# Optimization experiments

Hardware: AMD Instinct MI355X
Metric: run time of the kernel (lower is better)

## Reference

```python
import jax, jax.numpy as jnp
import numpy as np

B, F, C, W_, H_ = 4, 8, 256, 7, 7   # batch, frames, compressed channels (in_dim//r), width, height
CIN = 2048                          # in_dim
CH = CIN // 16                      # in_dim // (2*r) = 128, per-branch q/k channels


def _pw2d(x, W, b):
    # 1x1 Conv2d == per-pixel channel matmul. x: (N,Cin,H,W), W: (Cout,Cin)
    return jnp.einsum('nchw,oc->nohw', x, W) + b[None, :, None, None]


def setup_inputs() -> dict:
    key = jax.random.key(0)
    ks = iter(jax.random.split(key, 40))
    def rn(shape, s=0.02):
        return jax.random.normal(next(ks), shape, dtype=jnp.float32) * s
    inp = {
        'x':       rn((B * F, CIN, H_, W_), 1.0),
        'domainX': rn((B * F, CIN, H_, W_), 1.0),
        'domainY': rn((B * F, 1, H_, W_), 1.0),
        # conv1_1_pre (1 -> 2048), output is discarded in forward but computed faithfully
        'w_pre': rn((CIN, 1)), 'b_pre': rn((CIN,)),
        # conv3 (2048 -> 256); its weight is SHARED with layer1_downconv and layer1_downconv_Y
        'w_conv3': rn((C, CIN)), 'b_conv3': rn((C,)),
        # value_conv 1x1x1 Conv3d (256 -> 2048); weight SHARED with layer1_upconv(_Y)
        'w_value': rn((CIN, C)), 'b_value': rn((CIN,)),
        # tied-weight convs have their own biases
        'b_l1down': rn((C,)), 'b_l1up': rn((CIN,)),
        'b_l1down_Y': rn((C,)), 'b_l1up_Y': rn((CIN,)),
        # layer2 convs: independent weights (layer2_*gamma init to 0, so init add is a no-op)
        'w_l2down': rn((C, CIN)), 'b_l2down': rn((C,)),
        'w_l2up': rn((CIN, C)), 'b_l2up': rn((CIN,)),
        'w_l2down_Y': rn((C, CIN)), 'b_l2down_Y': rn((C,)),
        'w_l2up_Y': rn((CIN, C)), 'b_l2up_Y': rn((CIN,)),
        # q/k projections (2048 -> 128 each)
        'w_c11': rn((CH, CIN)), 'b_c11': rn((CH,)),
        'w_c12': rn((CH, CIN)), 'b_c12': rn((CH,)),
        'w_c21': rn((CH, CIN)), 'b_c21': rn((CH,)),
        'w_c22': rn((CH, CIN)), 'b_c22': rn((CH,)),
        'pos_embedV': rn((1, F, C * H_ * W_), 1.0),
        'gamma': jnp.asarray(0.01, dtype=jnp.float32),
    }
    return inp


def reference(x, domainX, domainY, w_pre, b_pre, w_conv3, b_conv3, w_value, b_value,
              b_l1down, b_l1up, b_l1down_Y, b_l1up_Y,
              w_l2down, b_l2down, w_l2up, b_l2up,
              w_l2down_Y, b_l2down_Y, w_l2up_Y, b_l2up_Y,
              w_c11, b_c11, w_c12, b_c12, w_c21, b_c21, w_c22, b_c22,
              pos_embedV, gamma):
    S = F * W_ * H_  # 392 tokens per clip
    # conv1_1_pre output is overwritten in the original forward (dead computation)
    _dead = _pw2d(domainY, w_pre, b_pre)
    del _dead
    # domainY path: down(conv3 weight) -> up(value_conv weight) -> layer2 down -> layer2 up
    # (create5D/create4D + permutes + 1x1x1 conv3d collapse to pointwise channel matmuls)
    dY = _pw2d(_pw2d(_pw2d(_pw2d(domainX, w_conv3, b_l1down_Y), w_value, b_l1up_Y),
                     w_l2down_Y, b_l2down_Y), w_l2up_Y, b_l2up_Y)
    q4 = jnp.concatenate([_pw2d(x, w_c11, b_c11), _pw2d(dY, w_c12, b_c12)], axis=1)  # (32,256,7,7)
    q = q4.reshape(B, F, C, W_, H_).transpose(0, 1, 3, 4, 2).reshape(B, S, C)
    # domainX path (same structure, shared layer1 weights, its own biases)
    dX = _pw2d(_pw2d(_pw2d(_pw2d(domainX, w_conv3, b_l1down), w_value, b_l1up),
                     w_l2down, b_l2down), w_l2up, b_l2up)
    k4 = jnp.concatenate([_pw2d(x, w_c21, b_c21), _pw2d(dX, w_c22, b_c22)], axis=1)
    k5 = k4.reshape(B, F, C, W_, H_).transpose(0, 1, 3, 4, 2)        # (B,F,W,H,C)
    k = k5.transpose(0, 2, 1, 3, 4).reshape(B, C, S)                 # faithful odd permute
    # value: conv3 -> +pos_embed -> rearrange to (B, S, C)
    v4 = _pw2d(x, w_conv3, b_conv3)                                  # (32,256,7,7)
    v = v4.reshape(B, F, C * W_ * H_) + pos_embedV                   # dropout p=0 is identity
    v = v.reshape(B, F, C, W_, H_).transpose(0, 1, 3, 4, 2).reshape(B, S, C)
    attn = jax.nn.softmax(jnp.einsum('bnc,bcm->bnm', q, k), axis=-1)  # (B,392,392)
    out = jnp.einsum('bnm,bmc->bnc', attn, v)
    out = out.reshape(B, F, W_, H_, C).transpose(0, 4, 1, 2, 3)      # (B,C,F,W,H)
    out = jnp.einsum('bcthw,oc->bothw', out, w_value) + b_value[None, :, None, None, None]
    out = out.transpose(0, 2, 1, 3, 4).reshape(B * F, CIN, W_, H_)
    return (gamma * out + x) * out + x
```

## Files before the change

### kernel.cpp

```cpp
#include <hip/hip_runtime.h>
#include <hip/hip_bf16.h>


typedef __attribute__((ext_vector_type(8))) short short8;
typedef __attribute__((ext_vector_type(4))) float f32x4;

#define TOKENS 1568

__device__ __forceinline__ ushort f2bf(float f) {
    uint32_t u = __float_as_uint(f);
    u += 0x7fffu + ((u >> 16) & 1u);
    return (ushort)(u >> 16);
}
__device__ __forceinline__ float bf2f(ushort h) { return __uint_as_float(((uint32_t)h) << 16); }
__device__ __forceinline__ void split2(float v, ushort& h, ushort& l) {
    h = f2bf(v); l = f2bf(v - bf2f(h));
}

__device__ __forceinline__ void gl16(const void* g, void* l) {
    __builtin_amdgcn_global_load_lds(
        (const __attribute__((address_space(1))) unsigned int*)g,
        (__attribute__((address_space(3))) unsigned int*)l, 16, 0, 0);
}

#define EPI_PART  0
#define EPI_BF16  1
#define EPI_SPLIT 2
#define EPI_FINAL 3

struct GA {
    const ushort *Ah, *Al; int lda; long sA;
    const ushort *Wh, *Wl; int ldw; long sW;
    const float* bias; int sB;
    int nkc, Kc;
    float* fO; ushort *bO, *bO2;
    int ldc; long sC; int M, N;
    int nx, ny;
    const float *ex, *gamma; float* fout;
};

template<int EPI, int SPL>
__device__ __forceinline__ void gmm_body(const GA g, int bx, int by, int bzf,
    ushort* LA_h, ushort* LW_h, ushort* LA_l, ushort* LW_l)
{
    constexpr bool HASL = (SPL >= 1);
    const int tid = threadIdx.x;
    const int bz = bzf / g.nkc;
    const int kc = bzf % g.nkc;
    const int row0 = by * 64, col0 = bx * 128;
    const bool sp = (SPL == 1) || (SPL == 2 && bx < 2);

    const int srow = tid >> 2;
    const int sq   = (tid & 3) ^ (srow & 3);
    int am  = row0 + srow;      if (am  > g.M - 1) am  = g.M - 1;
    int wn0 = col0 + srow;      if (wn0 > g.N - 1) wn0 = g.N - 1;
    int wn1 = col0 + 64 + srow; if (wn1 > g.N - 1) wn1 = g.N - 1;
    const long kbase = (long)kc * g.Kc + sq * 8;
    const ushort* gA  = g.Ah + bz * g.sA + (long)am  * g.lda + kbase;
    const ushort* gW0 = g.Wh + bz * g.sW + (long)wn0 * g.ldw + kbase;
    const ushort* gW1 = g.Wh + bz * g.sW + (long)wn1 * g.ldw + kbase;
    const ushort *gAl = nullptr, *gWl0 = nullptr, *gWl1 = nullptr;
    if constexpr (HASL) {
        if (sp) {
            gAl  = g.Al + bz * g.sA + (long)am  * g.lda + kbase;
            gWl0 = g.Wl + bz * g.sW + (long)wn0 * g.ldw + kbase;
            gWl1 = g.Wl + bz * g.sW + (long)wn1 * g.ldw + kbase;
        }
    }
    const int wb = (tid & 192) * 8;

    auto STAGE = [&](int buf, int k0) {
        gl16(gA + k0, LA_h + buf * 2048 + wb);
        gl16(gW0 + k0, LW_h + buf * 4096 + wb);
        gl16(gW1 + k0, LW_h + buf * 4096 + 2048 + wb);
        if constexpr (HASL) {
            if (sp) {
                gl16(gAl + k0, LA_l + buf * 2048 + wb);
                gl16(gWl0 + k0, LW_l + buf * 4096 + wb);
                gl16(gWl1 + k0, LW_l + buf * 4096 + 2048 + wb);
            }
        }
    };

    const int lane = tid & 63, wv = tid >> 6;
    const int wr = (wv >> 1) * 32, wc = (wv & 1) * 64;
    const int fr = lane & 15;
    const int ksw = ((lane >> 4) ^ (lane & 3)) * 8;
    int aoff[2], boff[4];
#pragma unroll
    for (int mi = 0; mi < 2; ++mi) aoff[mi] = (wr + mi * 16 + fr) * 32 + ksw;
#pragma unroll
    for (int ni = 0; ni < 4; ++ni) boff[ni] = (wc + ni * 16 + fr) * 32 + ksw;

    f32x4 acc[2][4];
#pragma unroll
    for (int mi = 0; mi < 2; ++mi)
#pragma unroll
        for (int ni = 0; ni < 4; ++ni) acc[mi][ni] = (f32x4){0.f, 0.f, 0.f, 0.f};

    STAGE(0, 0);
    __syncthreads();
    int cur = 0;
    for (int k0 = 0; k0 < g.Kc; k0 += 32) {
        if (k0 + 32 < g.Kc) STAGE(cur ^ 1, k0 + 32);

        short8 fa[2], fb[4];
#pragma unroll
        for (int mi = 0; mi < 2; ++mi) fa[mi] = *(const short8*)&LA_h[cur * 2048 + aoff[mi]];
#pragma unroll
        for (int ni = 0; ni < 4; ++ni) fb[ni] = *(const short8*)&LW_h[cur * 4096 + boff[ni]];
#pragma unroll
        for (int mi = 0; mi < 2; ++mi)
#pragma unroll
            for (int ni = 0; ni < 4; ++ni)
                acc[mi][ni] = __builtin_amdgcn_mfma_f32_16x16x32_bf16(fa[mi], fb[ni], acc[mi][ni], 0, 0, 0);
        if constexpr (HASL) {
            if (sp) {
                short8 ga[2], gb[4];
#pragma unroll
                for (int mi = 0; mi < 2; ++mi) ga[mi] = *(const short8*)&LA_l[cur * 2048 + aoff[mi]];
#pragma unroll
                for (int ni = 0; ni < 4; ++ni) gb[ni] = *(const short8*)&LW_l[cur * 4096 + boff[ni]];
#pragma unroll
                for (int mi = 0; mi < 2; ++mi)
#pragma unroll
                    for (int ni = 0; ni < 4; ++ni) {
                        acc[mi][ni] = __builtin_amdgcn_mfma_f32_16x16x32_bf16(fa[mi], gb[ni], acc[mi][ni], 0, 0, 0);
                        acc[mi][ni] = __builtin_amdgcn_mfma_f32_16x16x32_bf16(ga[mi], fb[ni], acc[mi][ni], 0, 0, 0);
                    }
            }
        }
        __syncthreads();
        cur ^= 1;
    }

    const int q4 = (lane >> 4) * 4;
    float gg = 0.f;
    if constexpr (EPI == EPI_FINAL) gg = g.gamma[0];
#pragma unroll
    for (int mi = 0; mi < 2; ++mi)
#pragma unroll
        for (int ni = 0; ni < 4; ++ni)
#pragma unroll
            for (int qi = 0; qi < 4; ++qi) {
                int m = row0 + wr + mi * 16 + q4 + qi;
                int n = col0 + wc + ni * 16 + fr;
                if (m >= g.M || n >= g.N) continue;
                float v = acc[mi][ni][qi];
                if (g.bias) v += g.bias[bz * g.sB + n];
                if constexpr (EPI == EPI_PART) {
                    g.fO[(long)bzf * g.sC + (long)m * g.ldc + n] = v;
                } else if constexpr (EPI == EPI_BF16) {
                    g.bO[(long)bzf * g.sC + (long)m * g.ldc + n] = f2bf(v);
                } else if constexpr (EPI == EPI_SPLIT) {
                    long o = (long)bzf * g.sC + (long)m * g.ldc + n;
                    ushort h, l; split2(v, h, l);
                    g.bO[o] = h; g.bO2[o] = l;
                } else {
                    int nimg = m / 49, p = m % 49;
                    long xi = (long)nimg * (2048 * 49) + (long)n * 49 + p;
                    float xv = g.ex[xi];
                    g.fout[xi] = (gg * v + xv) * v + xv;
                }
            }
}

template<int EPI, int SPL>
__global__ __launch_bounds__(256)
void gmm(GA g)
{
    __shared__ __align__(16) ushort LAh[2 * 2048], LWh[2 * 4096];
    __shared__ __align__(16) ushort LAl[(SPL >= 1) ? 2 * 2048 : 8];
    __shared__ __align__(16) ushort LWl[(SPL >= 1) ? 2 * 4096 : 8];
    gmm_body<EPI, SPL>(g, blockIdx.x, blockIdx.y, blockIdx.z, LAh, LWh, LAl, LWl);
}

template<int E1, int S1, int E2, int S2, int E3, int S3>
__global__ __launch_bounds__(256)
void gmm3(GA g1, int n1, GA g2, int n2, GA g3)
{
    __shared__ __align__(16) ushort LAh[2 * 2048], LWh[2 * 4096];
    __shared__ __align__(16) ushort LAl[2 * 2048], LWl[2 * 4096];
    int id = blockIdx.x;
    if (id < n1) {
        int bx = id % g1.nx, t = id / g1.nx;
        gmm_body<E1, S1>(g1, bx, t % g1.ny, t / g1.ny, LAh, LWh, LAl, LWl);
    } else if (id < n1 + n2) {
        id -= n1;
        int bx = id % g2.nx, t = id / g2.nx;
        gmm_body<E2, S2>(g2, bx, t % g2.ny, t / g2.ny, LAh, LWh, LAl, LWl);
    } else {
        id -= n1 + n2;
        int bx = id % g3.nx, t = id / g3.nx;
        gmm_body<E3, S3>(g3, bx, t % g3.ny, t / g3.ny, LAh, LWh, LAl, LWl);
    }
}

__global__ __launch_bounds__(256)
void prep(const float* c11, const float* c21, const float* conv3,
          const float* c22, const float* c12, const float* wval,
          const float* w2dX, const float* w2dY,
          const float* b_c11, const float* b_c21, const float* b_conv3,
          const float* x, const float* dX,
          const float* w2u, const float* w2uY, const float* wv, const float* w3,
          ushort* Wg1h, ushort* Wg1l, ushort* C2h, ushort* C2l, ushort* Wvalb,
          ushort* W2dSh, ushort* W2dSl, float* bg1,
          ushort* Xth, ushort* Xtl, ushort* DXth, ushort* DXtl,
          ushort* W2uTh, ushort* W2uTl, ushort* WvTh, ushort* WvTl,
          ushort* W3Th, ushort* W3Tl)
{
    __shared__ float tile[64][65];
    int b = blockIdx.x;
    int tid = threadIdx.x;
    if (b < 12290) {
        int e = b * 256 + tid;
        if (e < 1048576) {
            float v = e < 262144 ? c11[e] : e < 524288 ? c21[e - 262144] : conv3[e - 524288];
            ushort h, l; split2(v, h, l); Wg1h[e] = h; Wg1l[e] = l;
        } else if (e < 1572864) {
            int i = e - 1048576;
            float v = i < 262144 ? c22[i] : c12[i - 262144];
            ushort h, l; split2(v, h, l); C2h[i] = h; C2l[i] = l;
        } else if (e < 2097152) {
            int i = e - 1572864; Wvalb[i] = f2bf(wval[i]);
        } else if (e < 2097664) {
            int i = e - 2097152;
            bg1[i] = i < 128 ? b_c11[i] : i < 256 ? b_c21[i - 128] : b_conv3[i - 256];
        } else {
            int i = e - 2097664;
            float v = i < 524288 ? w2dX[i] : w2dY[i - 524288];
            ushort h, l; split2(v, h, l); W2dSh[i] = h; W2dSl[i] = l;
        }
    } else if (b < 14338) {
        int local = b - 12290;
        int z = local >> 10;
        int rem = local & 1023;
        int n = rem & 31, c0 = (rem >> 5) * 64;
        const float* src = z ? dX : x;
        ushort* oh = z ? DXth : Xth;
        ushort* ol = z ? DXtl : Xtl;
        const float* s = src + (long)n * (2048 * 49) + (long)c0 * 49;
        for (int idx = tid; idx < 64 * 49; idx += 256)
            tile[idx / 49][idx % 49] = s[idx];
        __syncthreads();
        for (int idx = tid; idx < 49 * 64; idx += 256) {
            int p = idx >> 6, cl = idx & 63;
            float v = tile[cl][p];
            long o = (long)(n * 49 + p) * 2048 + c0 + cl;
            ushort h, l; split2(v, h, l);
            oh[o] = h; ol[o] = l;
        }
    } else {
        int local = b - 14338;
        int zc = local >> 7, t = local & 127;
        const float* src; ushort *dh, *dl; int rows;
        switch (zc) {
            case 0:  src = w2u;  dh = W2uTh;          dl = W2uTl;          rows = 2048; break;
            case 1:  src = w2uY; dh = W2uTh + 524288; dl = W2uTl + 524288; rows = 2048; break;
            case 2:  src = wv;   dh = WvTh;           dl = WvTl;           rows = 2048; break;
            default: src = w3;   dh = W3Th;           dl = W3Tl;           rows = 256;  break;
        }
        int cols = 524288 / rows;
        int tilesX = cols >> 6;
        int tx = t % tilesX, ty = t / tilesX;
        for (int i = tid; i < 4096; i += 256) {
            int r = i >> 6, c = i & 63;
            tile[r][c] = src[(long)(ty * 64 + r) * cols + tx * 64 + c];
        }
        __syncthreads();
        for (int i = tid; i < 4096; i += 256) {
            int c = i >> 6, r = i & 63;
            float v = tile[r][c];
            ushort h, l; split2(v, h, l);
            long o = (long)(tx * 64 + c) * rows + ty * 64 + r;
            dh[o] = h; dl[o] = l;
        }
    }
}

__global__ __launch_bounds__(256)
void redA(const float* __restrict__ PG1, const float* __restrict__ bg1,
          const float* __restrict__ pos,
          ushort* Qh, ushort* Ql, ushort* KmH, ushort* KmL, ushort* Vh,
          const float* __restrict__ A1p, ushort* A1h, ushort* A1l,
          const float* __restrict__ Dp, ushort* DTh, ushort* DTl,
          const float* w2dX, const float* w2dY,
          const float* b1dX, const float* b1uX, const float* b2dX,
          const float* b1dY, const float* b1uY, const float* b2dY,
          float* __restrict__ dvec)
{
    int blk = blockIdx.x, tid = threadIdx.x;
    if (blk < 3136) {
        int idx = blk * 256 + tid;
        int m = idx >> 9, n = idx & 511;
        float v = bg1[n];
#pragma unroll
        for (int k = 0; k < 8; ++k) v += PG1[(long)k * 802816 + idx];
        int p = m % 49, img = m / 49;
        int f = img & 7, b = img >> 3;
        if (n < 128) {
            ushort h, l; split2(v, h, l);
            Qh[m * 256 + n] = h; Ql[m * 256 + n] = l;
        } else if (n < 256) {
            int c = n - 128;
            int flat = (p / 7) * 14336 + f * 1792 + (p % 7) * 256 + c;
            int ci = flat / 392, mm = flat % 392;
            long o = (long)b * 100352 + (long)mm * 256 + ci;
            ushort h, l; split2(v, h, l);
            KmH[o] = h; KmL[o] = l;
        } else {
            int c = n - 256;
            v += pos[f * 12544 + c * 49 + p];
            int s = m % 392;
            long o = (long)b * 106496 + (long)c * 416 + s;
            Vh[o] = f2bf(v);
            if (s < 24) Vh[o + 392] = 0;
        }
    } else if (blk < 3200) {
        int b2 = blk - 3136;
#pragma unroll
        for (int r = 0; r < 4; ++r) {
            int idx = b2 * 1024 + r * 256 + tid;
            int z = idx >> 15, e = idx & 32767;
            float v = 0.f;
#pragma unroll
            for (int k = 0; k < 8; ++k) v += A1p[(long)(z * 8 + k) * 32768 + e];
            ushort h, l; split2(v, h, l);
            A1h[idx] = h; A1l[idx] = l;
        }
    } else if (blk < 3232) {
        int b2 = blk - 3200;
#pragma unroll
        for (int r = 0; r < 16; ++r) {
            int idx = b2 * 4096 + r * 256 + tid;
            int z = idx >> 16, e = idx & 65535;
            int i = e >> 8, j = e & 255;
            float v = 0.f;
#pragma unroll
            for (int k = 0; k < 8; ++k) v += Dp[(long)(z * 8 + k) * 65536 + e];
            ushort h, l; split2(v, h, l);
            long o = (long)z * 65536 + (long)j * 256 + i;
            DTh[o] = h; DTl[o] = l;
        }
    } else {
        int blk2 = blk - 3232;
        int z = blk2 >> 6;
        int lane = tid & 63, wv = tid >> 6;
        int c = (blk2 & 63) * 4 + wv;
        const float* w2d = (z ? w2dY : w2dX) + (long)c * 2048;
        const float* b1d = z ? b1dY : b1dX;
        const float* b1u = z ? b1uY : b1uX;
        const float* b2d = z ? b2dY : b2dX;
        float acc = 0.f;
        for (int o = lane; o < 2048; o += 64) acc = fmaf(w2d[o], b1u[o], acc);
        for (int j = lane; j < 256; j += 64) {
            float d = 0.f;
#pragma unroll
            for (int k = 0; k < 8; ++k) d += Dp[(long)(z * 8 + k) * 65536 + (long)c * 256 + j];
            acc = fmaf(d, b1d[j], acc);
        }
        for (int off = 32; off; off >>= 1) acc += __shfl_down(acc, off, 64);
        if (lane == 0) dvec[z * 256 + c] = acc + b2d[c];
    }
}

__global__ __launch_bounds__(256)
void mkc(GA gM,
         const ushort* __restrict__ A1h, const ushort* __restrict__ A1l,
         const float* __restrict__ dvec,
         const float* c22, const float* c12,
         const float* b2uX, const float* b2uY,
         const float* bc22, const float* bc12, float* kc)
{
    __shared__ __align__(16) ushort LAh[2 * 2048], LWh[2 * 4096];
    __shared__ __align__(16) ushort LAl[2 * 2048], LWl[2 * 4096];
    int id = blockIdx.x;
    if (id < 64) {
        gmm_body<EPI_SPLIT, 1>(gM, id & 15, (id >> 4) & 1, id >> 5, LAh, LWh, LAl, LWl);
        return;
    }
    int tid = threadIdx.x, lane = tid & 63, wv = tid >> 6;
    int w = (id - 64) * 4 + wv;
    int z = w >> 7, i = w & 127;
    const ushort* a1h = A1h + (long)z * 32768 + i * 256;
    const ushort* a1l = A1h + (long)z * 32768 + i * 256;
    a1l = (const ushort*)((const ushort*)A1l + (long)z * 32768 + i * 256);
    const float* dv = dvec + z * 256;
    const float* cr = (z ? c12 : c22) + (long)i * 2048;
    const float* b2u = z ? b2uY : b2uX;
    float acc = 0.f;
    for (int c = lane; c < 256; c += 64)
        acc = fmaf(bf2f(a1h[c]) + bf2f(a1l[c]), dv[c], acc);
    for (int o = lane; o < 2048; o += 64) acc = fmaf(cr[o], b2u[o], acc);
    for (int off = 32; off; off >>= 1) acc += __shfl_down(acc, off, 64);
    if (lane == 0) kc[z * 128 + i] = acc + (z ? bc12 : bc22)[i];
}

__global__ __launch_bounds__(256)
void r_qk2(const float* __restrict__ P, const float* __restrict__ kc,
           ushort* Qh, ushort* Ql, ushort* KmH, ushort* KmL)
{
    int idx = blockIdx.x * 256 + threadIdx.x;
    int m = idx >> 8, j = idx & 255;
    float v = kc[j];
#pragma unroll
    for (int k = 0; k < 8; ++k) v += P[(long)k * 401408 + idx];
    ushort h, l; split2(v, h, l);
    if (j < 128) {
        int c = 128 + j;
        int p = m % 49, img = m / 49, f = img & 7, b = img >> 3;
        int flat = (p / 7) * 14336 + f * 1792 + (p % 7) * 256 + c;
        int ci = flat / 392, mm = flat % 392;
        long o = (long)b * 100352 + (long)mm * 256 + ci;
        KmH[o] = h; KmL[o] = l;
    } else {
        Qh[m * 256 + j] = h; Ql[m * 256 + j] = l;
    }
}

__global__ __launch_bounds__(256)
void fattn(const ushort* __restrict__ Qh, const ushort* __restrict__ Ql,
           const ushort* __restrict__ Kmh, const ushort* __restrict__ Kml,
           const ushort* __restrict__ VT, ushort* __restrict__ O)
{
    __shared__ float raw[16 * 420];
    __shared__ ushort P[16 * 424];
    const int b = blockIdx.y;
    const int r0 = blockIdx.x * 16;
    const int tid = threadIdx.x;
    const int lane = tid & 63, wv = tid >> 6;
    const int fr = lane & 15, g = lane >> 4;
    const int kb = g * 8;
    const long base = (long)b * 100352;
    const long vbase = (long)b * 106496;

    int qr = r0 + fr; if (qr > 391) qr = 391;
    const ushort* qph = Qh + base + (long)qr * 256 + kb;
    const ushort* qpl = Ql + base + (long)qr * 256 + kb;
    short8 qh[8], ql[8];
#pragma unroll
    for (int kf = 0; kf < 8; ++kf) {
        qh[kf] = *(const short8*)(qph + kf * 32);
        ql[kf] = *(const short8*)(qpl + kf * 32);
    }

    for (int nf = wv; nf < 26; nf += 4) {
        int kcol = nf * 16 + fr; if (kcol > 391) kcol = 391;
        const ushort* kph = Kmh + base + (long)kcol * 256 + kb;
        const ushort* kpl = Kml + base + (long)kcol * 256 + kb;
        f32x4 a = (f32x4){0.f, 0.f, 0.f, 0.f};
#pragma unroll
        for (int kf = 0; kf < 8; ++kf) {
            short8 bh = *(const short8*)(kph + kf * 32);
            short8 bl = *(const short8*)(kpl + kf * 32);
            a = __builtin_amdgcn_mfma_f32_16x16x32_bf16(qh[kf], bh, a, 0, 0, 0);
            a = __builtin_amdgcn_mfma_f32_16x16x32_bf16(qh[kf], bl, a, 0, 0, 0);
            a = __builtin_amdgcn_mfma_f32_16x16x32_bf16(ql[kf], bh, a, 0, 0, 0);
        }
#pragma unroll
        for (int q = 0; q < 4; ++q)
            raw[(g * 4 + q) * 420 + nf * 16 + fr] = a[q];
    }
    __syncthreads();

    {
        int row = tid >> 4, j = tid & 15;
        float v[26];
        float m = -1e30f;
#pragma unroll
        for (int k = 0; k < 26; ++k) {
            int col = j + 16 * k;
            v[k] = (col < 392) ? raw[row * 420 + col] : -1e30f;
            m = fmaxf(m, v[k]);
        }
#pragma unroll
        for (int off = 8; off; off >>= 1) m = fmaxf(m, __shfl_xor(m, off, 16));
        float s = 0.f;
#pragma unroll
        for (int k = 0; k < 26; ++k) { v[k] = __expf(v[k] - m); s += v[k]; }
#pragma unroll
        for (int off = 8; off; off >>= 1) s += __shfl_xor(s, off, 16);
        float inv = 1.f / s;
#pragma unroll
        for (int k = 0; k < 26; ++k) {
            int col = j + 16 * k;
            P[row * 424 + col] = (col < 392) ? f2bf(v[k] * inv) : (ushort)0;
        }
    }
    __syncthreads();

    const int cf0 = wv * 4;
    f32x4 o[4];
#pragma unroll
    for (int c = 0; c < 4; ++c) o[c] = (f32x4){0.f, 0.f, 0.f, 0.f};
#pragma unroll
    for (int kf = 0; kf < 13; ++kf) {
        short8 pa = *(const short8*)&P[fr * 424 + kf * 32 + kb];
#pragma unroll
        for (int c = 0; c < 4; ++c) {
            const ushort* vp = VT + vbase + (long)((cf0 + c) * 16 + fr) * 416 + kf * 32 + kb;
            short8 vb = *(const short8*)vp;
            o[c] = __builtin_amdgcn_mfma_f32_16x16x32_bf16(pa, vb, o[c], 0, 0, 0);
        }
    }
#pragma unroll
    for (int c = 0; c < 4; ++c)
#pragma unroll
        for (int q = 0; q < 4; ++q) {
            int orow = r0 + g * 4 + q;
            if (orow < 392)
                O[base + (long)orow * 256 + (cf0 + c) * 16 + fr] = f2bf(o[c][q]);
        }
}

extern "C" void kernel_launch(void* const* d_in, const int* in_sizes, int n_in,
                              void* d_out, int out_size, void* d_ws, size_t ws_size,
                              hipStream_t stream)
{
    const float* x        = (const float*)d_in[0];
    const float* domainX  = (const float*)d_in[1];
    const float* w_conv3  = (const float*)d_in[5];
    const float* b_conv3  = (const float*)d_in[6];
    const float* w_value  = (const float*)d_in[7];
    const float* b_value  = (const float*)d_in[8];
    const float* b_l1down   = (const float*)d_in[9];
    const float* b_l1up     = (const float*)d_in[10];
    const float* b_l1down_Y = (const float*)d_in[11];
    const float* b_l1up_Y   = (const float*)d_in[12];
    const float* w_l2down   = (const float*)d_in[13];
    const float* b_l2down   = (const float*)d_in[14];
    const float* w_l2up     = (const float*)d_in[15];
    const float* b_l2up     = (const float*)d_in[16];
    const float* w_l2down_Y = (const float*)d_in[17];
    const float* b_l2down_Y = (const float*)d_in[18];
    const float* w_l2up_Y   = (const float*)d_in[19];
    const float* b_l2up_Y   = (const float*)d_in[20];
    const float* w_c11 = (const float*)d_in[21];
    const float* b_c11 = (const float*)d_in[22];
    const float* w_c12 = (const float*)d_in[23];
    const float* b_c12 = (const float*)d_in[24];
    const float* w_c21 = (const float*)d_in[25];
    const float* b_c21 = (const float*)d_in[26];
    const float* w_c22 = (const float*)d_in[27];
    const float* b_c22 = (const float*)d_in[28];
    const float* pos   = (const float*)d_in[29];
    const float* gamma = (const float*)d_in[30];
    float* out = (float*)d_out;

    ushort* U = (ushort*)d_ws;
    float*  Fp = (float*)d_ws;

    const long oXt_h   = 0;
    const long oXt_l   = 3211264;
    const long oDXt_h  = 6422528;
    const long oDXt_l  = 9633792;
    const long oWg1_h  = 12845056;
    const long oWg1_l  = 13893632;
    const long oWval   = 14942208;
    const long oC2_h   = 15466496;
    const long oC2_l   = 15990784;
    const long oW2uT_h = 16515072;
    const long oW2uT_l = 17563648;
    const long oWvT_h  = 18612224;
    const long oWvT_l  = 19136512;
    const long oW3T_h  = 19660800;
    const long oW3T_l  = 20185088;
    const long oW2dS_h = 20709376;
    const long oW2dS_l = 21757952;
    const long oQ_h    = 22806528;
    const long oQ_l    = 23207936;
    const long oKm_h   = 23609344;
    const long oKm_l   = 24010752;
    const long oVT     = 24412160;
    const long oA1_h   = 24838144;
    const long oA1_l   = 24903680;
    const long oDT_h   = 24969216;
    const long oDT_l   = 25100288;
    const long oA3_h   = 25231360;
    const long oA3_l   = 25296896;
    const long oM_h    = 25362432;
    const long oM_l    = 25886720;
    const long oO      = 26411008;
    const long fPG1   = 13406208;
    const long fA1p   = 19828736;
    const long fDp    = 20353024;
    const long fPG2   = 21401600;
    const long fbg1   = 24612864;
    const long fkc    = 24613376;
    const long fdv    = 24613632;

    GA Z = {};

    prep<<<dim3(14850), 256, 0, stream>>>(
        w_c11, w_c21, w_conv3, w_c22, w_c12, w_value, w_l2down, w_l2down_Y,
        b_c11, b_c21, b_conv3, x, domainX,
        w_l2up, w_l2up_Y, w_value, w_conv3,
        U + oWg1_h, U + oWg1_l, U + oC2_h, U + oC2_l, U + oWval,
        U + oW2dS_h, U + oW2dS_l, Fp + fbg1,
        U + oXt_h, U + oXt_l, U + oDXt_h, U + oDXt_l,
        U + oW2uT_h, U + oW2uT_l, U + oWvT_h, U + oWvT_l,
        U + oW3T_h, U + oW3T_l);

    {
        GA g1 = Z;
        g1.Ah = U + oXt_h; g1.Al = U + oXt_l; g1.lda = 2048; g1.sA = 0;
        g1.Wh = U + oWg1_h; g1.Wl = U + oWg1_l; g1.ldw = 2048; g1.sW = 0;
        g1.nkc = 8; g1.Kc = 256; g1.fO = Fp + fPG1;
        g1.ldc = 512; g1.sC = 802816; g1.M = TOKENS; g1.N = 512; g1.nx = 4; g1.ny = 25;
        GA ga1 = Z;
        ga1.Ah = U + oC2_h; ga1.Al = U + oC2_l; ga1.lda = 2048; ga1.sA = 262144;
        ga1.Wh = U + oW2uT_h; ga1.Wl = U + oW2uT_l; ga1.ldw = 2048; ga1.sW = 524288;
        ga1.nkc = 8; ga1.Kc = 256; ga1.fO = Fp + fA1p;
        ga1.ldc = 256; ga1.sC = 32768; ga1.M = 128; ga1.N = 256; ga1.nx = 2; ga1.ny = 2;
        GA gd = Z;
        gd.Ah = U + oW2dS_h; gd.Al = U + oW2dS_l; gd.lda = 2048; gd.sA = 524288;
        gd.Wh = U + oWvT_h; gd.Wl = U + oWvT_l; gd.ldw = 2048; gd.sW = 0;
        gd.nkc = 8; gd.Kc = 256; gd.fO = Fp + fDp;
        gd.ldc = 256; gd.sC = 65536; gd.M = 256; gd.N = 256; gd.nx = 2; gd.ny = 4;
        gmm3<EPI_PART, 2, EPI_PART, 1, EPI_PART, 1><<<dim3(992), 256, 0, stream>>>(
            g1, 800, ga1, 64, gd);
    }

    redA<<<dim3(3360), 256, 0, stream>>>(Fp + fPG1, Fp + fbg1, pos,
        U + oQ_h, U + oQ_l, U + oKm_h, U + oKm_l, U + oVT,
        Fp + fA1p, U + oA1_h, U + oA1_l,
        Fp + fDp, U + oDT_h, U + oDT_l,
        w_l2down, w_l2down_Y,
        b_l1down, b_l1up, b_l2down,
        b_l1down_Y, b_l1up_Y, b_l2down_Y,
        Fp + fdv);

    {
        GA g = Z;
        g.Ah = U + oA1_h; g.Al = U + oA1_l; g.lda = 256; g.sA = 32768;
        g.Wh = U + oDT_h; g.Wl = U + oDT_l; g.ldw = 256; g.sW = 65536;
        g.nkc = 1; g.Kc = 256; g.bO = U + oA3_h; g.bO2 = U + oA3_l;
        g.ldc = 256; g.sC = 32768; g.M = 128; g.N = 256; g.nx = 2; g.ny = 2;
        gmm<EPI_SPLIT, 1><<<dim3(2, 2, 2), 256, 0, stream>>>(g);
    }

    {
        GA g = Z;
        g.Ah = U + oA3_h; g.Al = U + oA3_l; g.lda = 256; g.sA = 32768;
        g.Wh = U + oW3T_h; g.Wl = U + oW3T_l; g.ldw = 256; g.sW = 0;
        g.nkc = 1; g.Kc = 256; g.bO = U + oM_h; g.bO2 = U + oM_l;
        g.ldc = 2048; g.sC = 262144; g.M = 128; g.N = 2048; g.nx = 16; g.ny = 2;
        mkc<<<dim3(128), 256, 0, stream>>>(g,
            U + oA1_h, U + oA1_l, Fp + fdv,
            w_c22, w_c12, b_l2up, b_l2up_Y,
            b_c22, b_c12, Fp + fkc);
    }

    {
        GA g = Z;
        g.Ah = U + oDXt_h; g.Al = U + oDXt_l; g.lda = 2048; g.sA = 0;
        g.Wh = U + oM_h; g.Wl = U + oM_l; g.ldw = 2048; g.sW = 0;
        g.nkc = 8; g.Kc = 256; g.fO = Fp + fPG2;
        g.ldc = 256; g.sC = 401408; g.M = TOKENS; g.N = 256; g.nx = 2; g.ny = 25;
        gmm<EPI_PART, 1><<<dim3(2, 25, 8), 256, 0, stream>>>(g);
    }

    r_qk2<<<dim3(1568), 256, 0, stream>>>(Fp + fPG2, Fp + fkc,
        U + oQ_h, U + oQ_l, U + oKm_h, U + oKm_l);

    fattn<<<dim3(25, 4), 256, 0, stream>>>(
        U + oQ_h, U + oQ_l, U + oKm_h, U + oKm_l, U + oVT, U + oO);

    {
        GA g = Z;
        g.Ah = U + oO; g.Al = nullptr; g.lda = 256; g.sA = 0;
        g.Wh = U + oWval; g.Wl = nullptr; g.ldw = 256; g.sW = 0;
        g.bias = b_value; g.sB = 0;
        g.nkc = 1; g.Kc = 256;
        g.ldc = 0; g.sC = 0; g.M = TOKENS; g.N = 2048; g.nx = 16; g.ny = 25;
        g.ex = x; g.gamma = gamma; g.fout = out;
        gmm<EPI_FINAL, 0><<<dim3(16, 25, 1), 256, 0, stream>>>(g);
    }
}
```

Before: 170.6 us.

## Replace split-bf16 hi/lo emulation with single fp16 MFMA throughout pipeline

```diff
diff --git a/kernel.cpp b/kernel.cpp
--- a/kernel.cpp
+++ b/kernel.cpp
@@ -2,19 +2,18 @@
 #include <hip/hip_bf16.h>
 
 
-typedef __attribute__((ext_vector_type(8))) short short8;
+typedef __attribute__((ext_vector_type(8))) _Float16 half8;
 typedef __attribute__((ext_vector_type(4))) float f32x4;
 
 #define TOKENS 1568
 
-__device__ __forceinline__ ushort f2bf(float f) {
-    uint32_t u = __float_as_uint(f);
-    u += 0x7fffu + ((u >> 16) & 1u);
-    return (ushort)(u >> 16);
-}
-__device__ __forceinline__ float bf2f(ushort h) { return __uint_as_float(((uint32_t)h) << 16); }
-__device__ __forceinline__ void split2(float v, ushort& h, ushort& l) {
-    h = f2bf(v); l = f2bf(v - bf2f(h));
+__device__ __forceinline__ ushort f2h(float f) {
+    _Float16 h = (_Float16)f;
+    return *(ushort*)&h;
+}
+__device__ __forceinline__ float h2f(ushort u) {
+    _Float16 h = *(_Float16*)&u;
+    return (float)h;
 }
 
 __device__ __forceinline__ void gl16(const void* g, void* l) {
@@ -24,31 +23,28 @@
 }
 
 #define EPI_PART  0
-#define EPI_BF16  1
-#define EPI_SPLIT 2
-#define EPI_FINAL 3
+#define EPI_F16   1
+#define EPI_FINAL 2
 
 struct GA {
-    const ushort *Ah, *Al; int lda; long sA;
-    const ushort *Wh, *Wl; int ldw; long sW;
+    const ushort* Ah; int lda; long sA;
+    const ushort* Wh; int ldw; long sW;
     const float* bias; int sB;
     int nkc, Kc;
-    float* fO; ushort *bO, *bO2;
+    float* fO; ushort* bO;
     int ldc; long sC; int M, N;
     int nx, ny;
     const float *ex, *gamma; float* fout;
 };
 
-template<int EPI, int SPL>
+template<int EPI>
 __device__ __forceinline__ void gmm_body(const GA g, int bx, int by, int bzf,
-    ushort* LA_h, ushort* LW_h, ushort* LA_l, ushort* LW_l)
-{
-    constexpr bool HASL = (SPL >= 1);
+                                         ushort* LA, ushort* LW)
+{
     const int tid = threadIdx.x;
     const int bz = bzf / g.nkc;
     const int kc = bzf % g.nkc;
     const int row0 = by * 64, col0 = bx * 128;
-    const bool sp = (SPL == 1) || (SPL == 2 && bx < 2);
 
     const int srow = tid >> 2;
     const int sq   = (tid & 3) ^ (srow & 3);
@@ -59,27 +55,12 @@
     const ushort* gA  = g.Ah + bz * g.sA + (long)am  * g.lda + kbase;
     const ushort* gW0 = g.Wh + bz * g.sW + (long)wn0 * g.ldw + kbase;
     const ushort* gW1 = g.Wh + bz * g.sW + (long)wn1 * g.ldw + kbase;
-    const ushort *gAl = nullptr, *gWl0 = nullptr, *gWl1 = nullptr;
-    if constexpr (HASL) {
-        if (sp) {
-            gAl  = g.Al + bz * g.sA + (long)am  * g.lda + kbase;
-            gWl0 = g.Wl + bz * g.sW + (long)wn0 * g.ldw + kbase;
-            gWl1 = g.Wl + bz * g.sW + (long)wn1 * g.ldw + kbase;
-        }
-    }
     const int wb = (tid & 192) * 8;
 
     auto STAGE = [&](int buf, int k0) {
-        gl16(gA + k0, LA_h + buf * 2048 + wb);
-        gl16(gW0 + k0, LW_h + buf * 4096 + wb);
-        gl16(gW1 + k0, LW_h + buf * 4096 + 2048 + wb);
-        if constexpr (HASL) {
-            if (sp) {
-                gl16(gAl + k0, LA_l + buf * 2048 + wb);
-                gl16(gWl0 + k0, LW_l + buf * 4096 + wb);
-                gl16(gWl1 + k0, LW_l + buf * 4096 + 2048 + wb);
-            }
-        }
+        gl16(gA + k0, LA + buf * 2048 + wb);
+        gl16(gW0 + k0, LW + buf * 4096 + wb);
+        gl16(gW1 + k0, LW + buf * 4096 + 2048 + wb);
     };
 
     const int lane = tid & 63, wv = tid >> 6;
@@ -104,32 +85,16 @@
     for (int k0 = 0; k0 < g.Kc; k0 += 32) {
         if (k0 + 32 < g.Kc) STAGE(cur ^ 1, k0 + 32);
 
-        short8 fa[2], fb[4];
-#pragma unroll
-        for (int mi = 0; mi < 2; ++mi) fa[mi] = *(const short8*)&LA_h[cur * 2048 + aoff[mi]];
-#pragma unroll
-        for (int ni = 0; ni < 4; ++ni) fb[ni] = *(const short8*)&LW_h[cur * 4096 + boff[ni]];
+        half8 fa[2], fb[4];
+#pragma unroll
+        for (int mi = 0; mi < 2; ++mi) fa[mi] = *(half8*)&LA[cur * 2048 + aoff[mi]];
+#pragma unroll
+        for (int ni = 0; ni < 4; ++ni) fb[ni] = *(half8*)&LW[cur * 4096 + boff[ni]];
 #pragma unroll
         for (int mi = 0; mi < 2; ++mi)
 #pragma unroll
             for (int ni = 0; ni < 4; ++ni)
-                acc[mi][ni] = __builtin_amdgcn_mfma_f32_16x16x32_bf16(fa[mi], fb[ni], acc[mi][ni], 0, 0, 0);
-        if constexpr (HASL) {
-            if (sp) {
-                short8 ga[2], gb[4];
-#pragma unroll
-                for (int mi = 0; mi < 2; ++mi) ga[mi] = *(const short8*)&LA_l[cur * 2048 + aoff[mi]];
-#pragma unroll
-                for (int ni = 0; ni < 4; ++ni) gb[ni] = *(const short8*)&LW_l[cur * 4096 + boff[ni]];
-#pragma unroll
-                for (int mi = 0; mi < 2; ++mi)
-#pragma unroll
-                    for (int ni = 0; ni < 4; ++ni) {
-                        acc[mi][ni] = __builtin_amdgcn_mfma_f32_16x16x32_bf16(fa[mi], gb[ni], acc[mi][ni], 0, 0, 0);
-                        acc[mi][ni] = __builtin_amdgcn_mfma_f32_16x16x32_bf16(ga[mi], fb[ni], acc[mi][ni], 0, 0, 0);
-                    }
-            }
-        }
+                acc[mi][ni] = __builtin_amdgcn_mfma_f32_16x16x32_f16(fa[mi], fb[ni], acc[mi][ni], 0, 0, 0);
         __syncthreads();
         cur ^= 1;
     }
@@ -150,12 +115,8 @@
                 if (g.bias) v += g.bias[bz * g.sB + n];
                 if constexpr (EPI == EPI_PART) {
                     g.fO[(long)bzf * g.sC + (long)m * g.ldc + n] = v;
-                } else if constexpr (EPI == EPI_BF16) {
-                    g.bO[(long)bzf * g.sC + (long)m * g.ldc + n] = f2bf(v);
-                } else if constexpr (EPI == EPI_SPLIT) {
-                    long o = (long)bzf * g.sC + (long)m * g.ldc + n;
-                    ushort h, l; split2(v, h, l);
-                    g.bO[o] = h; g.bO2[o] = l;
+                } else if constexpr (EPI == EPI_F16) {
+                    g.bO[(long)bzf * g.sC + (long)m * g.ldc + n] = f2h(v);
                 } else {
                     int nimg = m / 49, p = m % 49;
                     long xi = (long)nimg * (2048 * 49) + (long)n * 49 + p;
@@ -165,34 +126,30 @@
             }
 }
 
-template<int EPI, int SPL>
+template<int EPI>
 __global__ __launch_bounds__(256)
 void gmm(GA g)
 {
-    __shared__ __align__(16) ushort LAh[2 * 2048], LWh[2 * 4096];
-    __shared__ __align__(16) ushort LAl[(SPL >= 1) ? 2 * 2048 : 8];
-    __shared__ __align__(16) ushort LWl[(SPL >= 1) ? 2 * 4096 : 8];
-    gmm_body<EPI, SPL>(g, blockIdx.x, blockIdx.y, blockIdx.z, LAh, LWh, LAl, LWl);
-}
-
-template<int E1, int S1, int E2, int S2, int E3, int S3>
+    __shared__ __align__(16) ushort LA[2 * 2048], LW[2 * 4096];
+    gmm_body<EPI>(g, blockIdx.x, blockIdx.y, blockIdx.z, LA, LW);
+}
+
 __global__ __launch_bounds__(256)
 void gmm3(GA g1, int n1, GA g2, int n2, GA g3)
 {
-    __shared__ __align__(16) ushort LAh[2 * 2048], LWh[2 * 4096];
-    __shared__ __align__(16) ushort LAl[2 * 2048], LWl[2 * 4096];
+    __shared__ __align__(16) ushort LA[2 * 2048], LW[2 * 4096];
     int id = blockIdx.x;
     if (id < n1) {
         int bx = id % g1.nx, t = id / g1.nx;
-        gmm_body<E1, S1>(g1, bx, t % g1.ny, t / g1.ny, LAh, LWh, LAl, LWl);
+        gmm_body<EPI_PART>(g1, bx, t % g1.ny, t / g1.ny, LA, LW);
     } else if (id < n1 + n2) {
         id -= n1;
         int bx = id % g2.nx, t = id / g2.nx;
-        gmm_body<E2, S2>(g2, bx, t % g2.ny, t / g2.ny, LAh, LWh, LAl, LWl);
+        gmm_body<EPI_PART>(g2, bx, t % g2.ny, t / g2.ny, LA, LW);
     } else {
         id -= n1 + n2;
         int bx = id % g3.nx, t = id / g3.nx;
-        gmm_body<E3, S3>(g3, bx, t % g3.ny, t / g3.ny, LAh, LWh, LAl, LWl);
+        gmm_body<EPI_PART>(g3, bx, t % g3.ny, t / g3.ny, LA, LW);
     }
 }
 
@@ -203,11 +160,9 @@
           const float* b_c11, const float* b_c21, const float* b_conv3,
           const float* x, const float* dX,
           const float* w2u, const float* w2uY, const float* wv, const float* w3,
-          ushort* Wg1h, ushort* Wg1l, ushort* C2h, ushort* C2l, ushort* Wvalb,
-          ushort* W2dSh, ushort* W2dSl, float* bg1,
-          ushort* Xth, ushort* Xtl, ushort* DXth, ushort* DXtl,
-          ushort* W2uTh, ushort* W2uTl, ushort* WvTh, ushort* WvTl,
-          ushort* W3Th, ushort* W3Tl)
+          ushort* Wg1, ushort* C2, ushort* Wval, ushort* W2dS, float* bg1,
+          ushort* Xt, ushort* DXt,
+          ushort* W2uT, ushort* WvT, ushort* W3T)
 {
     __shared__ float tile[64][65];
     int b = blockIdx.x;
@@ -216,20 +171,18 @@
         int e = b * 256 + tid;
         if (e < 1048576) {
             float v = e < 262144 ? c11[e] : e < 524288 ? c21[e - 262144] : conv3[e - 524288];
-            ushort h, l; split2(v, h, l); Wg1h[e] = h; Wg1l[e] = l;
+            Wg1[e] = f2h(v);
         } else if (e < 1572864) {
             int i = e - 1048576;
-            float v = i < 262144 ? c22[i] : c12[i - 262144];
-            ushort h, l; split2(v, h, l); C2h[i] = h; C2l[i] = l;
+            C2[i] = f2h(i < 262144 ? c22[i] : c12[i - 262144]);
         } else if (e < 2097152) {
-            int i = e - 1572864; Wvalb[i] = f2bf(wval[i]);
+            int i = e - 1572864; Wval[i] = f2h(wval[i]);
         } else if (e < 2097664) {
             int i = e - 2097152;
             bg1[i] = i < 128 ? b_c11[i] : i < 256 ? b_c21[i - 128] : b_conv3[i - 256];
         } else {
             int i = e - 2097664;
-            float v = i < 524288 ? w2dX[i] : w2dY[i - 524288];
-            ushort h, l; split2(v, h, l); W2dSh[i] = h; W2dSl[i] = l;
+            W2dS[i] = f2h(i < 524288 ? w2dX[i] : w2dY[i - 524288]);
         }
     } else if (b < 14338) {
         int local = b - 12290;
@@ -237,28 +190,25 @@
         int rem = local & 1023;
         int n = rem & 31, c0 = (rem >> 5) * 64;
         const float* src = z ? dX : x;
-        ushort* oh = z ? DXth : Xth;
-        ushort* ol = z ? DXtl : Xtl;
+        ushort* oh = z ? DXt : Xt;
         const float* s = src + (long)n * (2048 * 49) + (long)c0 * 49;
         for (int idx = tid; idx < 64 * 49; idx += 256)
             tile[idx / 49][idx % 49] = s[idx];
         __syncthreads();
         for (int idx = tid; idx < 49 * 64; idx += 256) {
             int p = idx >> 6, cl = idx & 63;
-            float v = tile[cl][p];
             long o = (long)(n * 49 + p) * 2048 + c0 + cl;
-            ushort h, l; split2(v, h, l);
-            oh[o] = h; ol[o] = l;
+            oh[o] = f2h(tile[cl][p]);
         }
     } else {
         int local = b - 14338;
         int zc = local >> 7, t = local & 127;
-        const float* src; ushort *dh, *dl; int rows;
+        const float* src; ushort* dh; int rows;
         switch (zc) {
-            case 0:  src = w2u;  dh = W2uTh;          dl = W2uTl;          rows = 2048; break;
-            case 1:  src = w2uY; dh = W2uTh + 524288; dl = W2uTl + 524288; rows = 2048; break;
-            case 2:  src = wv;   dh = WvTh;           dl = WvTl;           rows = 2048; break;
-            default: src = w3;   dh = W3Th;           dl = W3Tl;           rows = 256;  break;
+            case 0:  src = w2u;  dh = W2uT;          rows = 2048; break;
+            case 1:  src = w2uY; dh = W2uT + 524288; rows = 2048; break;
+            case 2:  src = wv;   dh = WvT;           rows = 2048; break;
+            default: src = w3;   dh = W3T;           rows = 256;  break;
         }
         int cols = 524288 / rows;
         int tilesX = cols >> 6;
@@ -270,10 +220,8 @@
         __syncthreads();
         for (int i = tid; i < 4096; i += 256) {
             int c = i >> 6, r = i & 63;
-            float v = tile[r][c];
-            ushort h, l; split2(v, h, l);
             long o = (long)(tx * 64 + c) * rows + ty * 64 + r;
-            dh[o] = h; dl[o] = l;
+            dh[o] = f2h(tile[r][c]);
         }
     }
 }
@@ -281,9 +229,9 @@
 __global__ __launch_bounds__(256)
 void redA(const float* __restrict__ PG1, const float* __restrict__ bg1,
           const float* __restrict__ pos,
-          ushort* Qh, ushort* Ql, ushort* KmH, ushort* KmL, ushort* Vh,
-          const float* __restrict__ A1p, ushort* A1h, ushort* A1l,
-          const float* __restrict__ Dp, ushort* DTh, ushort* DTl,
+          ushort* Q, ushort* Km, ushort* V,
+          const float* __restrict__ A1p, ushort* A1,
+          const float* __restrict__ Dp, ushort* DT,
           const float* w2dX, const float* w2dY,
           const float* b1dX, const float* b1uX, const float* b2dX,
           const float* b1dY, const float* b1uY, const float* b2dY,
@@ -299,22 +247,19 @@
         int p = m % 49, img = m / 49;
         int f = img & 7, b = img >> 3;
         if (n < 128) {
-            ushort h, l; split2(v, h, l);
-            Qh[m * 256 + n] = h; Ql[m * 256 + n] = l;
+            Q[m * 256 + n] = f2h(v);
         } else if (n < 256) {
             int c = n - 128;
             int flat = (p / 7) * 14336 + f * 1792 + (p % 7) * 256 + c;
             int ci = flat / 392, mm = flat % 392;
-            long o = (long)b * 100352 + (long)mm * 256 + ci;
-            ushort h, l; split2(v, h, l);
-            KmH[o] = h; KmL[o] = l;
+            Km[(long)b * 100352 + (long)mm * 256 + ci] = f2h(v);
         } else {
             int c = n - 256;
             v += pos[f * 12544 + c * 49 + p];
             int s = m % 392;
             long o = (long)b * 106496 + (long)c * 416 + s;
-            Vh[o] = f2bf(v);
-            if (s < 24) Vh[o + 392] = 0;
+            V[o] = f2h(v);
+            if (s < 24) V[o + 392] = 0;
         }
     } else if (blk < 3200) {
         int b2 = blk - 3136;
@@ -325,8 +270,7 @@
             float v = 0.f;
 #pragma unroll
             for (int k = 0; k < 8; ++k) v += A1p[(long)(z * 8 + k) * 32768 + e];
-            ushort h, l; split2(v, h, l);
-            A1h[idx] = h; A1l[idx] = l;
+            A1[idx] = f2h(v);
         }
     } else if (blk < 3232) {
         int b2 = blk - 3200;
@@ -338,9 +282,7 @@
             float v = 0.f;
 #pragma unroll
             for (int k = 0; k < 8; ++k) v += Dp[(long)(z * 8 + k) * 65536 + e];
-            ushort h, l; split2(v, h, l);
-            long o = (long)z * 65536 + (long)j * 256 + i;
-            DTh[o] = h; DTl[o] = l;
+            DT[(long)z * 65536 + (long)j * 256 + i] = f2h(v);
         }
     } else {
         int blk2 = blk - 3232;
@@ -366,31 +308,26 @@
 
 __global__ __launch_bounds__(256)
 void mkc(GA gM,
-         const ushort* __restrict__ A1h, const ushort* __restrict__ A1l,
-         const float* __restrict__ dvec,
+         const ushort* __restrict__ A1, const float* __restrict__ dvec,
          const float* c22, const float* c12,
          const float* b2uX, const float* b2uY,
          const float* bc22, const float* bc12, float* kc)
 {
-    __shared__ __align__(16) ushort LAh[2 * 2048], LWh[2 * 4096];
-    __shared__ __align__(16) ushort LAl[2 * 2048], LWl[2 * 4096];
+    __shared__ __align__(16) ushort LA[2 * 2048], LW[2 * 4096];
     int id = blockIdx.x;
     if (id < 64) {
-        gmm_body<EPI_SPLIT, 1>(gM, id & 15, (id >> 4) & 1, id >> 5, LAh, LWh, LAl, LWl);
+        gmm_body<EPI_F16>(gM, id & 15, (id >> 4) & 1, id >> 5, LA, LW);
         return;
     }
     int tid = threadIdx.x, lane = tid & 63, wv = tid >> 6;
     int w = (id - 64) * 4 + wv;
     int z = w >> 7, i = w & 127;
-    const ushort* a1h = A1h + (long)z * 32768 + i * 256;
-    const ushort* a1l = A1h + (long)z * 32768 + i * 256;
-    a1l = (const ushort*)((const ushort*)A1l + (long)z * 32768 + i * 256);
+    const ushort* a1 = A1 + (long)z * 32768 + i * 256;
     const float* dv = dvec + z * 256;
     const float* cr = (z ? c12 : c22) + (long)i * 2048;
     const float* b2u = z ? b2uY : b2uX;
     float acc = 0.f;
-    for (int c = lane; c < 256; c += 64)
-        acc = fmaf(bf2f(a1h[c]) + bf2f(a1l[c]), dv[c], acc);
+    for (int c = lane; c < 256; c += 64) acc = fmaf(h2f(a1[c]), dv[c], acc);
     for (int o = lane; o < 2048; o += 64) acc = fmaf(cr[o], b2u[o], acc);
     for (int off = 32; off; off >>= 1) acc += __shfl_down(acc, off, 64);
     if (lane == 0) kc[z * 128 + i] = acc + (z ? bc12 : bc22)[i];
@@ -398,29 +335,27 @@
 
 __global__ __launch_bounds__(256)
 void r_qk2(const float* __restrict__ P, const float* __restrict__ kc,
-           ushort* Qh, ushort* Ql, ushort* KmH, ushort* KmL)
+           ushort* Q, ushort* Km)
 {
     int idx = blockIdx.x * 256 + threadIdx.x;
     int m = idx >> 8, j = idx & 255;
     float v = kc[j];
 #pragma unroll
     for (int k = 0; k < 8; ++k) v += P[(long)k * 401408 + idx];
-    ushort h, l; split2(v, h, l);
+    ushort h = f2h(v);
     if (j < 128) {
         int c = 128 + j;
         int p = m % 49, img = m / 49, f = img & 7, b = img >> 3;
         int flat = (p / 7) * 14336 + f * 1792 + (p % 7) * 256 + c;
         int ci = flat / 392, mm = flat % 392;
-        long o = (long)b * 100352 + (long)mm * 256 + ci;
-        KmH[o] = h; KmL[o] = l;
+        Km[(long)b * 100352 + (long)mm * 256 + ci] = h;
     } else {
-        Qh[m * 256 + j] = h; Ql[m * 256 + j] = l;
-    }
-}
-
-__global__ __launch_bounds__(256)
-void fattn(const ushort* __restrict__ Qh, const ushort* __restrict__ Ql,
-           const ushort* __restrict__ Kmh, const ushort* __restrict__ Kml,
+        Q[m * 256 + j] = h;
+    }
+}
+
+__global__ __launch_bounds__(256)
+void fattn(const ushort* __restrict__ Qg, const ushort* __restrict__ Kmg,
            const ushort* __restrict__ VT, ushort* __restrict__ O)
 {
     __shared__ float raw[16 * 420];
@@ -435,27 +370,19 @@
     const long vbase = (long)b * 106496;
 
     int qr = r0 + fr; if (qr > 391) qr = 391;
-    const ushort* qph = Qh + base + (long)qr * 256 + kb;
-    const ushort* qpl = Ql + base + (long)qr * 256 + kb;
-    short8 qh[8], ql[8];
-#pragma unroll
-    for (int kf = 0; kf < 8; ++kf) {
-        qh[kf] = *(const short8*)(qph + kf * 32);
-        ql[kf] = *(const short8*)(qpl + kf * 32);
-    }
+    const ushort* qp = Qg + base + (long)qr * 256 + kb;
+    half8 qh[8];
+#pragma unroll
+    for (int kf = 0; kf < 8; ++kf) qh[kf] = *(const half8*)(qp + kf * 32);
 
     for (int nf = wv; nf < 26; nf += 4) {
         int kcol = nf * 16 + fr; if (kcol > 391) kcol = 391;
-        const ushort* kph = Kmh + base + (long)kcol * 256 + kb;
-        const ushort* kpl = Kml + base + (long)kcol * 256 + kb;
+        const ushort* kp = Kmg + base + (long)kcol * 256 + kb;
         f32x4 a = (f32x4){0.f, 0.f, 0.f, 0.f};
 #pragma unroll
         for (int kf = 0; kf < 8; ++kf) {
-            short8 bh = *(const short8*)(kph + kf * 32);
-            short8 bl = *(const short8*)(kpl + kf * 32);
-            a = __builtin_amdgcn_mfma_f32_16x16x32_bf16(qh[kf], bh, a, 0, 0, 0);
-            a = __builtin_amdgcn_mfma_f32_16x16x32_bf16(qh[kf], bl, a, 0, 0, 0);
-            a = __builtin_amdgcn_mfma_f32_16x16x32_bf16(ql[kf], bh, a, 0, 0, 0);
+            half8 bh = *(const half8*)(kp + kf * 32);
+            a = __builtin_amdgcn_mfma_f32_16x16x32_f16(qh[kf], bh, a, 0, 0, 0);
         }
 #pragma unroll
         for (int q = 0; q < 4; ++q)
@@ -484,7 +411,7 @@
 #pragma unroll
         for (int k = 0; k < 26; ++k) {
             int col = j + 16 * k;
-            P[row * 424 + col] = (col < 392) ? f2bf(v[k] * inv) : (ushort)0;
+            P[row * 424 + col] = (col < 392) ? f2h(v[k] * inv) : (ushort)0;
         }
     }
     __syncthreads();
@@ -495,12 +422,12 @@
     for (int c = 0; c < 4; ++c) o[c] = (f32x4){0.f, 0.f, 0.f, 0.f};
 #pragma unroll
     for (int kf = 0; kf < 13; ++kf) {
-        short8 pa = *(const short8*)&P[fr * 424 + kf * 32 + kb];
+        half8 pa = *(half8*)&P[fr * 424 + kf * 32 + kb];
 #pragma unroll
         for (int c = 0; c < 4; ++c) {
             const ushort* vp = VT + vbase + (long)((cf0 + c) * 16 + fr) * 416 + kf * 32 + kb;
-            short8 vb = *(const short8*)vp;
-            o[c] = __builtin_amdgcn_mfma_f32_16x16x32_bf16(pa, vb, o[c], 0, 0, 0);
+            half8 vb = *(const half8*)vp;
+            o[c] = __builtin_amdgcn_mfma_f32_16x16x32_f16(pa, vb, o[c], 0, 0, 0);
         }
     }
 #pragma unroll
@@ -509,7 +436,7 @@
         for (int q = 0; q < 4; ++q) {
             int orow = r0 + g * 4 + q;
             if (orow < 392)
-                O[base + (long)orow * 256 + (cf0 + c) * 16 + fr] = f2bf(o[c][q]);
+                O[base + (long)orow * 256 + (cf0 + c) * 16 + fr] = f2h(o[c][q]);
         }
 }
 
@@ -550,44 +477,30 @@
     ushort* U = (ushort*)d_ws;
     float*  Fp = (float*)d_ws;
 
-    const long oXt_h   = 0;
-    const long oXt_l   = 3211264;
-    const long oDXt_h  = 6422528;
-    const long oDXt_l  = 9633792;
-    const long oWg1_h  = 12845056;
-    const long oWg1_l  = 13893632;
-    const long oWval   = 14942208;
-    const long oC2_h   = 15466496;
-    const long oC2_l   = 15990784;
-    const long oW2uT_h = 16515072;
-    const long oW2uT_l = 17563648;
-    const long oWvT_h  = 18612224;
-    const long oWvT_l  = 19136512;
-    const long oW3T_h  = 19660800;
-    const long oW3T_l  = 20185088;
-    const long oW2dS_h = 20709376;
-    const long oW2dS_l = 21757952;
-    const long oQ_h    = 22806528;
-    const long oQ_l    = 23207936;
-    const long oKm_h   = 23609344;
-    const long oKm_l   = 24010752;
-    const long oVT     = 24412160;
-    const long oA1_h   = 24838144;
-    const long oA1_l   = 24903680;
-    const long oDT_h   = 24969216;
-    const long oDT_l   = 25100288;
-    const long oA3_h   = 25231360;
-    const long oA3_l   = 25296896;
-    const long oM_h    = 25362432;
-    const long oM_l    = 25886720;
-    const long oO      = 26411008;
-    const long fPG1   = 13406208;
-    const long fA1p   = 19828736;
-    const long fDp    = 20353024;
-    const long fPG2   = 21401600;
-    const long fbg1   = 24612864;
-    const long fkc    = 24613376;
-    const long fdv    = 24613632;
+    const long oXt   = 0;
+    const long oDXt  = 3211264;
+    const long oWg1  = 6422528;
+    const long oWval = 7471104;
+    const long oC2   = 7995392;
+    const long oW2uT = 8519680;
+    const long oWvT  = 9568256;
+    const long oW3T  = 10092544;
+    const long oW2dS = 10616832;
+    const long oQ    = 11665408;
+    const long oKm   = 12066816;
+    const long oVT   = 12468224;
+    const long oA1   = 12894208;
+    const long oDT   = 12959744;
+    const long oA3   = 13090816;
+    const long oM    = 13156352;
+    const long oO    = 13680640;
+    const long fPG1  = 7041024;
+    const long fA1p  = 13463552;
+    const long fDp   = 13987840;
+    const long fPG2  = 15036416;
+    const long fbg1  = 18247680;
+    const long fkc   = 18248192;
+    const long fdv   = 18248448;
 
     GA Z = {};
 
@@ -595,36 +508,33 @@
         w_c11, w_c21, w_conv3, w_c22, w_c12, w_value, w_l2down, w_l2down_Y,
         b_c11, b_c21, b_conv3, x, domainX,
         w_l2up, w_l2up_Y, w_value, w_conv3,
-        U + oWg1_h, U + oWg1_l, U + oC2_h, U + oC2_l, U + oWval,
-        U + oW2dS_h, U + oW2dS_l, Fp + fbg1,
-        U + oXt_h, U + oXt_l, U + oDXt_h, U + oDXt_l,
-        U + oW2uT_h, U + oW2uT_l, U + oWvT_h, U + oWvT_l,
-        U + oW3T_h, U + oW3T_l);
+        U + oWg1, U + oC2, U + oWval, U + oW2dS, Fp + fbg1,
+        U + oXt, U + oDXt,
+        U + oW2uT, U + oWvT, U + oW3T);
 
     {
         GA g1 = Z;
-        g1.Ah = U + oXt_h; g1.Al = U + oXt_l; g1.lda = 2048; g1.sA = 0;
-        g1.Wh = U + oWg1_h; g1.Wl = U + oWg1_l; g1.ldw = 2048; g1.sW = 0;
+        g1.Ah = U + oXt; g1.lda = 2048; g1.sA = 0;
+        g1.Wh = U + oWg1; g1.ldw = 2048; g1.sW = 0;
         g1.nkc = 8; g1.Kc = 256; g1.fO = Fp + fPG1;
         g1.ldc = 512; g1.sC = 802816; g1.M = TOKENS; g1.N = 512; g1.nx = 4; g1.ny = 25;
         GA ga1 = Z;
-        ga1.Ah = U + oC2_h; ga1.Al = U + oC2_l; ga1.lda = 2048; ga1.sA = 262144;
-        ga1.Wh = U + oW2uT_h; ga1.Wl = U + oW2uT_l; ga1.ldw = 2048; ga1.sW = 524288;
+        ga1.Ah = U + oC2; ga1.lda = 2048; ga1.sA = 262144;
+        ga1.Wh = U + oW2uT; ga1.ldw = 2048; ga1.sW = 524288;
         ga1.nkc = 8; ga1.Kc = 256; ga1.fO = Fp + fA1p;
         ga1.ldc = 256; ga1.sC = 32768; ga1.M = 128; ga1.N = 256; ga1.nx = 2; ga1.ny = 2;
         GA gd = Z;
-        gd.Ah = U + oW2dS_h; gd.Al = U + oW2dS_l; gd.lda = 2048; gd.sA = 524288;
-        gd.Wh = U + oWvT_h; gd.Wl = U + oWvT_l; gd.ldw = 2048; gd.sW = 0;
+        gd.Ah = U + oW2dS; gd.lda = 2048; gd.sA = 524288;
+        gd.Wh = U + oWvT; gd.ldw = 2048; gd.sW = 0;
         gd.nkc = 8; gd.Kc = 256; gd.fO = Fp + fDp;
         gd.ldc = 256; gd.sC = 65536; gd.M = 256; gd.N = 256; gd.nx = 2; gd.ny = 4;
-        gmm3<EPI_PART, 2, EPI_PART, 1, EPI_PART, 1><<<dim3(992), 256, 0, stream>>>(
-            g1, 800, ga1, 64, gd);
+        gmm3<<<dim3(992), 256, 0, stream>>>(g1, 800, ga1, 64, gd);
     }
 
     redA<<<dim3(3360), 256, 0, stream>>>(Fp + fPG1, Fp + fbg1, pos,
-        U + oQ_h, U + oQ_l, U + oKm_h, U + oKm_l, U + oVT,
-        Fp + fA1p, U + oA1_h, U + oA1_l,
-        Fp + fDp, U + oDT_h, U + oDT_l,
+        U + oQ, U + oKm, U + oVT,
+        Fp + fA1p, U + oA1,
+        Fp + fDp, U + oDT,
         w_l2down, w_l2down_Y,
         b_l1down, b_l1up, b_l2down,
         b_l1down_Y, b_l1up_Y, b_l2down_Y,
@@ -632,48 +542,46 @@
 
     {
         GA g = Z;
-        g.Ah = U + oA1_h; g.Al = U + oA1_l; g.lda = 256; g.sA = 32768;
-        g.Wh = U + oDT_h; g.Wl = U + oDT_l; g.ldw = 256; g.sW = 65536;
-        g.nkc = 1; g.Kc = 256; g.bO = U + oA3_h; g.bO2 = U + oA3_l;
+        g.Ah = U + oA1; g.lda = 256; g.sA = 32768;
+        g.Wh = U + oDT; g.ldw = 256; g.sW = 65536;
+        g.nkc = 1; g.Kc = 256; g.bO = U + oA3;
         g.ldc = 256; g.sC = 32768; g.M = 128; g.N = 256; g.nx = 2; g.ny = 2;
-        gmm<EPI_SPLIT, 1><<<dim3(2, 2, 2), 256, 0, stream>>>(g);
+        gmm<EPI_F16><<<dim3(2, 2, 2), 256, 0, stream>>>(g);
     }
 
     {
         GA g = Z;
-        g.Ah = U + oA3_h; g.Al = U + oA3_l; g.lda = 256; g.sA = 32768;
-        g.Wh = U + oW3T_h; g.Wl = U + oW3T_l; g.ldw = 256; g.sW = 0;
-        g.nkc = 1; g.Kc = 256; g.bO = U + oM_h; g.bO2 = U + oM_l;
+        g.Ah = U + oA3; g.lda = 256; g.sA = 32768;
+        g.Wh = U + oW3T; g.ldw = 256; g.sW = 0;
+        g.nkc = 1; g.Kc = 256; g.bO = U + oM;
         g.ldc = 2048; g.sC = 262144; g.M = 128; g.N = 2048; g.nx = 16; g.ny = 2;
         mkc<<<dim3(128), 256, 0, stream>>>(g,
-            U + oA1_h, U + oA1_l, Fp + fdv,
+            U + oA1, Fp + fdv,
             w_c22, w_c12, b_l2up, b_l2up_Y,
             b_c22, b_c12, Fp + fkc);
     }
 
     {
         GA g = Z;
-        g.Ah = U + oDXt_h; g.Al = U + oDXt_l; g.lda = 2048; g.sA = 0;
-        g.Wh = U + oM_h; g.Wl = U + oM_l; g.ldw = 2048; g.sW = 0;
+        g.Ah = U + oDXt; g.lda = 2048; g.sA = 0;
+        g.Wh = U + oM; g.ldw = 2048; g.sW = 0;
         g.nkc = 8; g.Kc = 256; g.fO = Fp + fPG2;
         g.ldc = 256; g.sC = 401408; g.M = TOKENS; g.N = 256; g.nx = 2; g.ny = 25;
-        gmm<EPI_PART, 1><<<dim3(2, 25, 8), 256, 0, stream>>>(g);
-    }
-
-    r_qk2<<<dim3(1568), 256, 0, stream>>>(Fp + fPG2, Fp + fkc,
-        U + oQ_h, U + oQ_l, U + oKm_h, U + oKm_l);
-
-    fattn<<<dim3(25, 4), 256, 0, stream>>>(
-        U + oQ_h, U + oQ_l, U + oKm_h, U + oKm_l, U + oVT, U + oO);
+        gmm<EPI_PART><<<dim3(2, 25, 8), 256, 0, stream>>>(g);
+    }
+
+    r_qk2<<<dim3(1568), 256, 0, stream>>>(Fp + fPG2, Fp + fkc, U + oQ, U + oKm);
+
+    fattn<<<dim3(25, 4), 256, 0, stream>>>(U + oQ, U + oKm, U + oVT, U + oO);
 
     {
         GA g = Z;
-        g.Ah = U + oO; g.Al = nullptr; g.lda = 256; g.sA = 0;
-        g.Wh = U + oWval; g.Wl = nullptr; g.ldw = 256; g.sW = 0;
+        g.Ah = U + oO; g.lda = 256; g.sA = 0;
+        g.Wh = U + oWval; g.ldw = 256; g.sW = 0;
         g.bias = b_value; g.sB = 0;
         g.nkc = 1; g.Kc = 256;
         g.ldc = 0; g.sC = 0; g.M = TOKENS; g.N = 2048; g.nx = 16; g.ny = 25;
         g.ex = x; g.gamma = gamma; g.fout = out;
-        gmm<EPI_FINAL, 0><<<dim3(16, 25, 1), 256, 0, stream>>>(g);
-    }
-}
+        gmm<EPI_FINAL><<<dim3(16, 25, 1), 256, 0, stream>>>(g);
+    }
+}
```

After: 149.3 us. -12.5%, faster.
